# Optimization experiments

Measured on AMD Instinct MI355X. Metric: run time of the kernel, lower is better.

The kernel has to match this reference:

```python
import jax, jax.numpy as jnp
import numpy as np

B, CF, CG, CI = 2, 64, 64, 32
D = H = W = 64

def setup_inputs() -> dict:
    key = jax.random.key(0)
    k1, k2, k3, k4, k5 = jax.random.split(key, 5)
    x = jax.random.normal(k1, (B, CF, D, H, W), dtype=jnp.float32)
    g = jax.random.normal(k2, (B, CG, D, H, W), dtype=jnp.float32)
    # 1x1x1 conv weights reduce to [out_ch, in_ch]; kaiming-like scale
    Wg = jax.random.normal(k3, (CI, CG), dtype=jnp.float32) * (1.0 / np.sqrt(CG))
    Wx = jax.random.normal(k4, (CI, CF), dtype=jnp.float32) * (1.0 / np.sqrt(CF))
    Wpsi = jax.random.normal(k5, (1, CI), dtype=jnp.float32) * (1.0 / np.sqrt(CI))
    return {"x": x, "g": g, "Wg": Wg, "Wx": Wx, "Wpsi": Wpsi}

def reference(x, g, Wg, Wx, Wpsi):
    # 1x1x1 Conv3d == per-voxel matmul over channel dim
    g1 = jnp.einsum('oc,bcdhw->bodhw', Wg, g)          # [B,CI,D,H,W]
    x1 = jnp.einsum('oc,bcdhw->bodhw', Wx, x)          # [B,CI,D,H,W]
    a = jax.nn.relu(g1 + x1)
    psi = jnp.einsum('oc,bcdhw->bodhw', Wpsi, a)       # [B,1,D,H,W]
    psi = jax.nn.sigmoid(psi)
    return x * psi                                      # broadcast over CF
```

## Files before the change

kernel.cpp:

```cpp
#include <hip/hip_runtime.h>


#define SPAT 262144
#define NVOX 524288
#define CIN  64
#define COUT 32
#define S2   (SPAT / 2)

typedef float v2f __attribute__((ext_vector_type(2)));

__global__ __launch_bounds__(256) void transpose_w(const float* __restrict__ Wg,
                                                   const float* __restrict__ Wx,
                                                   float* __restrict__ Wcat) {
    int idx = blockIdx.x * 256 + threadIdx.x;
    int c = idx >> 6;
    int o = idx & 63;
    float v = (o < 32) ? Wg[o * CIN + c] : Wx[(o - 32) * CIN + c];
    Wcat[c * 64 + o] = v;
}

__global__ __launch_bounds__(256, 4) void gate_main(const v2f* __restrict__ x,
                                                    const v2f* __restrict__ g,
                                                    const float* __restrict__ Wcat,
                                                    const float* __restrict__ Wpsi,
                                                    v2f* __restrict__ out) {
    int p = blockIdx.x * 256 + threadIdx.x;
    int b = p >> 17;
    int s = p & (S2 - 1);

    const v2f* __restrict__ xp = x + (size_t)b * CIN * S2 + s;
    const v2f* __restrict__ gp = g + (size_t)b * CIN * S2 + s;

    v2f acc[COUT];
#pragma unroll
    for (int o = 0; o < COUT; ++o) acc[o] = (v2f)(0.0f);

#pragma unroll 2
    for (int c = 0; c < CIN; ++c) {
        v2f gc = __builtin_nontemporal_load(gp + (size_t)c * S2);
        v2f xc = xp[(size_t)c * S2];
        const float* w = Wcat + c * 64;
#pragma unroll
        for (int o = 0; o < COUT; ++o) {
            float wg = w[o], wx = w[32 + o];
            acc[o].x = fmaf(wg, gc.x, fmaf(wx, xc.x, acc[o].x));
            acc[o].y = fmaf(wg, gc.y, fmaf(wx, xc.y, acc[o].y));
        }
    }

    float px = 0.0f, py = 0.0f;
#pragma unroll
    for (int o = 0; o < COUT; ++o) {
        float wp = Wpsi[o];
        px = fmaf(wp, fmaxf(acc[o].x, 0.0f), px);
        py = fmaf(wp, fmaxf(acc[o].y, 0.0f), py);
    }
    float psix = 1.0f / (1.0f + __expf(-px));
    float psiy = 1.0f / (1.0f + __expf(-py));

    v2f* __restrict__ op = out + (size_t)b * CIN * S2 + s;
#pragma unroll 4
    for (int c = 0; c < CIN; ++c) {
        v2f xv = xp[(size_t)c * S2];
        v2f ov; ov.x = xv.x * psix; ov.y = xv.y * psiy;
        __builtin_nontemporal_store(ov, op + (size_t)c * S2);
    }
}

extern "C" void kernel_launch(void* const* d_in, const int* in_sizes, int n_in,
                              void* d_out, int out_size, void* d_ws, size_t ws_size,
                              hipStream_t stream) {
    const float* x    = (const float*)d_in[0];
    const float* g    = (const float*)d_in[1];
    const float* Wg   = (const float*)d_in[2];
    const float* Wx   = (const float*)d_in[3];
    const float* Wpsi = (const float*)d_in[4];
    float* out  = (float*)d_out;
    float* Wcat = (float*)d_ws;

    transpose_w<<<16, 256, 0, stream>>>(Wg, Wx, Wcat);
    gate_main<<<NVOX / 2 / 256, 256, 0, stream>>>((const v2f*)x, (const v2f*)g,
                                                  Wcat, Wpsi, (v2f*)out);
}
```

Measured before the change: 322.6 us.

## Stage channel chunks through LDS with 16-byte loads and stores

Each block now handles a 512-voxel tile. It stages 8-channel chunks of x and g into shared memory using 128-bit loads, and computes the 2-voxel-per-thread dot products from LDS. The sigmoid gate is shared through LDS, so the final x*psi pass can use 128-bit row-wise loads and stores with each wave covering 16 channels. The aim is wider, fully coalesced global accesses in place of 8-byte strided ones, at the cost of extra __syncthreads and about 33 KB of LDS per block, which may limit occupancy.

```diff
diff --git a/kernel.cpp b/kernel.cpp
--- a/kernel.cpp
+++ b/kernel.cpp
@@ -5,9 +5,11 @@
 #define NVOX 524288
 #define CIN  64
 #define COUT 32
-#define S2   (SPAT / 2)
+#define TILE 512
+#define CH   8
 
 typedef float v2f __attribute__((ext_vector_type(2)));
+typedef float v4f __attribute__((ext_vector_type(4)));
 
 __global__ __launch_bounds__(256) void transpose_w(const float* __restrict__ Wg,
                                                    const float* __restrict__ Wx,
@@ -19,51 +21,84 @@
     Wcat[c * 64 + o] = v;
 }
 
-__global__ __launch_bounds__(256, 4) void gate_main(const v2f* __restrict__ x,
-                                                    const v2f* __restrict__ g,
+__global__ __launch_bounds__(256, 4) void gate_main(const float* __restrict__ x,
+                                                    const float* __restrict__ g,
                                                     const float* __restrict__ Wcat,
                                                     const float* __restrict__ Wpsi,
-                                                    v2f* __restrict__ out) {
-    int p = blockIdx.x * 256 + threadIdx.x;
-    int b = p >> 17;
-    int s = p & (S2 - 1);
+                                                    float* __restrict__ out) {
+    __shared__ float xs[CH][TILE];
+    __shared__ float gs[CH][TILE];
+    __shared__ float psis[TILE];
 
-    const v2f* __restrict__ xp = x + (size_t)b * CIN * S2 + s;
-    const v2f* __restrict__ gp = g + (size_t)b * CIN * S2 + s;
+    int tid = threadIdx.x;
+    int v0 = blockIdx.x * TILE;
+    int b = v0 >> 18;
+    int s0 = v0 & (SPAT - 1);
+
+    const float* __restrict__ xb = x + (size_t)b * CIN * SPAT + s0;
+    const float* __restrict__ gb = g + (size_t)b * CIN * SPAT + s0;
+    float* __restrict__ ob = out + (size_t)b * CIN * SPAT + s0;
 
     v2f acc[COUT];
 #pragma unroll
     for (int o = 0; o < COUT; ++o) acc[o] = (v2f)(0.0f);
 
-#pragma unroll 2
-    for (int c = 0; c < CIN; ++c) {
-        v2f gc = __builtin_nontemporal_load(gp + (size_t)c * S2);
-        v2f xc = xp[(size_t)c * S2];
-        const float* w = Wcat + c * 64;
+#pragma unroll 1
+    for (int c0 = 0; c0 < CIN; c0 += CH) {
+        if (c0) __syncthreads();
+
 #pragma unroll
-        for (int o = 0; o < COUT; ++o) {
-            float wg = w[o], wx = w[32 + o];
-            acc[o].x = fmaf(wg, gc.x, fmaf(wx, xc.x, acc[o].x));
-            acc[o].y = fmaf(wg, gc.y, fmaf(wx, xc.y, acc[o].y));
+        for (int j = 0; j < 4; ++j) {
+            int idx = j * 256 + tid;
+            int ch = idx >> 7;
+            int col = idx & 127;
+            v4f xv = *((const v4f*)(xb + (size_t)(c0 + ch) * SPAT) + col);
+            v4f gv = __builtin_nontemporal_load(
+                         (const v4f*)(gb + (size_t)(c0 + ch) * SPAT) + col);
+            *((v4f*)&xs[ch][0] + col) = xv;
+            *((v4f*)&gs[ch][0] + col) = gv;
+        }
+        __syncthreads();
+
+#pragma unroll
+        for (int cc = 0; cc < CH; ++cc) {
+            v2f xc = *((const v2f*)&xs[cc][0] + tid);
+            v2f gc = *((const v2f*)&gs[cc][0] + tid);
+            const float* w = Wcat + (c0 + cc) * 64;
+#pragma unroll
+            for (int o = 0; o < COUT; ++o) {
+                float wg = w[o], wx = w[32 + o];
+                acc[o].x = fmaf(wg, gc.x, fmaf(wx, xc.x, acc[o].x));
+                acc[o].y = fmaf(wg, gc.y, fmaf(wx, xc.y, acc[o].y));
+            }
         }
     }
 
-    float px = 0.0f, py = 0.0f;
+    float psx = 0.0f, psy = 0.0f;
 #pragma unroll
     for (int o = 0; o < COUT; ++o) {
         float wp = Wpsi[o];
-        px = fmaf(wp, fmaxf(acc[o].x, 0.0f), px);
-        py = fmaf(wp, fmaxf(acc[o].y, 0.0f), py);
+        psx = fmaf(wp, fmaxf(acc[o].x, 0.0f), psx);
+        psy = fmaf(wp, fmaxf(acc[o].y, 0.0f), psy);
     }
-    float psix = 1.0f / (1.0f + __expf(-px));
-    float psiy = 1.0f / (1.0f + __expf(-py));
+    v2f psi;
+    psi.x = 1.0f / (1.0f + __expf(-psx));
+    psi.y = 1.0f / (1.0f + __expf(-psy));
+    *((v2f*)psis + tid) = psi;
+    __syncthreads();
 
-    v2f* __restrict__ op = out + (size_t)b * CIN * S2 + s;
-#pragma unroll 4
-    for (int c = 0; c < CIN; ++c) {
-        v2f xv = xp[(size_t)c * S2];
-        v2f ov; ov.x = xv.x * psix; ov.y = xv.y * psiy;
-        __builtin_nontemporal_store(ov, op + (size_t)c * S2);
+    int w = tid >> 6, l = tid & 63;
+    v4f p0 = *((const v4f*)psis + l);
+    v4f p1 = *((const v4f*)psis + 64 + l);
+#pragma unroll 1
+    for (int i = 0; i < 16; ++i) {
+        int c = w * 16 + i;
+        const v4f* __restrict__ xr = (const v4f*)(xb + (size_t)c * SPAT);
+        v4f* __restrict__ orow = (v4f*)(ob + (size_t)c * SPAT);
+        v4f x0 = xr[l];
+        v4f x1 = xr[64 + l];
+        __builtin_nontemporal_store(x0 * p0, orow + l);
+        __builtin_nontemporal_store(x1 * p1, orow + 64 + l);
     }
 }
 
@@ -79,6 +114,5 @@
     float* Wcat = (float*)d_ws;
 
     transpose_w<<<16, 256, 0, stream>>>(Wg, Wx, Wcat);
-    gate_main<<<NVOX / 2 / 256, 256, 0, stream>>>((const v2f*)x, (const v2f*)g,
-                                                  Wcat, Wpsi, (v2f*)out);
+    gate_main<<<NVOX / TILE, 256, 0, stream>>>(x, g, Wcat, Wpsi, out);
 }
```

New measurement: 370.2 us. 1.15x slower.
